# Performance work log

Hardware: AMD Instinct MI355X
Metric: run time of the kernel (lower is better)

The kernel has to match this reference:

```python
import jax, jax.numpy as jnp
import numpy as np

N = 50000      # num_nodes
E = 800000     # num_edges (before self-loops)
IN = 512       # in_channels
HID = 64       # hidden_channels
H = 8          # num_heads (layer 1)
OUT = 128      # out_channels
NEG_SLOPE = 0.2


def setup_inputs() -> dict:
    key = jax.random.key(0)
    ks = jax.random.split(key, 10)
    x = jax.random.normal(ks[0], (N, IN), jnp.float32)
    edge_index = jax.random.randint(ks[1], (2, E), 0, N, jnp.int32)

    def glorot(k, shape):
        fan_in, fan_out = shape[0], int(np.prod(shape[1:]))
        s = jnp.sqrt(2.0 / (fan_in + fan_out)).astype(jnp.float32)
        return jax.random.normal(k, shape, jnp.float32) * s

    # layer 1: GATConv(IN -> HID, heads=H, concat=True)
    W1 = glorot(ks[2], (IN, H * HID))
    att_src1 = glorot(ks[3], (H, HID))
    att_dst1 = glorot(ks[4], (H, HID))
    b1 = jnp.zeros((H * HID,), jnp.float32)
    # layer 2: GATConv(H*HID -> OUT, heads=1, concat=False)
    W2 = glorot(ks[5], (H * HID, OUT))
    att_src2 = glorot(ks[6], (1, OUT))
    att_dst2 = glorot(ks[7], (1, OUT))
    b2 = jnp.zeros((OUT,), jnp.float32)
    return {"x": x, "edge_index": edge_index,
            "W1": W1, "b1": b1, "att_src1": att_src1, "att_dst1": att_dst1,
            "W2": W2, "b2": b2, "att_src2": att_src2, "att_dst2": att_dst2}


def gat_layer(x, src, dst, W, b, a_src, a_dst, heads, concat):
    n = x.shape[0]
    h = (x @ W).reshape(n, heads, -1)                     # [N, H, C]
    e_src = (h * a_src).sum(-1)                           # [N, H]
    e_dst = (h * a_dst).sum(-1)                           # [N, H]
    e = jax.nn.leaky_relu(e_src[src] + e_dst[dst], NEG_SLOPE)   # [E, H]
    # segment softmax over incoming edges of each destination node
    m = jax.ops.segment_max(e, dst, num_segments=n)       # [N, H]
    m = jnp.where(jnp.isneginf(m), 0.0, m)                # empty segments
    p = jnp.exp(e - m[dst])                               # [E, H]
    s = jax.ops.segment_sum(p, dst, num_segments=n)       # [N, H]
    alpha = p / (s[dst] + 1e-16)                          # [E, H]
    out = jax.ops.segment_sum(alpha[..., None] * h[src], dst, num_segments=n)  # [N, H, C]
    if concat:
        return out.reshape(n, -1) + b
    return out.mean(axis=1) + b


def reference(x, edge_index, W1, b1, att_src1, att_dst1, W2, b2, att_src2, att_dst2):
    # PyG GATConv adds self-loops by default
    loops = jnp.arange(N, dtype=edge_index.dtype)
    src = jnp.concatenate([edge_index[0], loops])
    dst = jnp.concatenate([edge_index[1], loops])
    h = gat_layer(x, src, dst, W1, b1, att_src1, att_dst1, H, True)   # [N, H*HID]
    h = jax.nn.relu(h)
    out = gat_layer(h, src, dst, W2, b2, att_src2, att_dst2, 1, False)  # [N, OUT]
    return out
```

## Files before the change

### kernel.cpp

```cpp
#include <hip/hip_runtime.h>
#include <hip/hip_fp16.h>

#define NNODES 50000
#define NEDGES 800000
#define ETOT   (NNODES + NEDGES)
#define NH     8
#define HID    64
#define D1     512
#define INC    512
#define OUTC   128
#define NEG    0.2f
#define MPAD   50048

typedef __attribute__((ext_vector_type(8))) short short8;
typedef __attribute__((ext_vector_type(4))) float f32x4;
typedef _Float16 half8v __attribute__((ext_vector_type(8)));
typedef _Float16 half2v __attribute__((ext_vector_type(2)));

__device__ __forceinline__ ushort f2h_bits(float x) {
    _Float16 h = (_Float16)x; return __builtin_bit_cast(ushort, h);
}
__device__ __forceinline__ float h2f(ushort b) {
    return (float)__builtin_bit_cast(_Float16, b);
}
__device__ __forceinline__ uint splat_h2(float p) {
    uint b = (uint)f2h_bits(p); return b | (b << 16);
}
__device__ __forceinline__ half2v as_h2(uint u) { return __builtin_bit_cast(half2v, u); }
__device__ __forceinline__ float leaky(float v) { return v >= 0.f ? v : NEG * v; }

__global__ void count_deg(const int* __restrict__ ei, int* __restrict__ deg) {
    int i = blockIdx.x * 256 + threadIdx.x;
    if (i >= ETOT) return;
    int dst = (i < NEDGES) ? ei[NEDGES + i] : (i - NEDGES);
    atomicAdd(&deg[dst], 1);
}

__global__ void scan_deg(const int* __restrict__ deg, int* __restrict__ rs) {
    __shared__ int part[1024];
    const int n = NNODES;
    const int CH = (n + 1023) / 1024;
    int t = threadIdx.x;
    int lo = t * CH, hi = min(lo + CH, n);
    int s = 0;
    for (int i = lo; i < hi; ++i) s += deg[i];
    part[t] = s;
    __syncthreads();
    for (int off = 1; off < 1024; off <<= 1) {
        int v = (t >= off) ? part[t - off] : 0;
        __syncthreads();
        part[t] += v;
        __syncthreads();
    }
    int run = (t == 0) ? 0 : part[t - 1];
    for (int i = lo; i < hi; ++i) { rs[i] = run; run += deg[i]; }
    if (hi == n) rs[n] = run;
}

__global__ void scatter_edges(const int* __restrict__ ei, int* __restrict__ cursor,
                              int* __restrict__ csr_src) {
    int i = blockIdx.x * 256 + threadIdx.x;
    if (i >= ETOT) return;
    int src, dst;
    if (i < NEDGES) { src = ei[i]; dst = ei[NEDGES + i]; }
    else            { src = dst = i - NEDGES; }
    int pos = atomicAdd(&cursor[dst], 1);
    csr_src[pos] = src;
}

__global__ void cast_f16(const float* __restrict__ x, ushort* __restrict__ xh, int n4) {
    int i = blockIdx.x * 256 + threadIdx.x;
    if (i >= n4) return;
    float4 v = *(const float4*)&x[(size_t)i * 4];
    ushort4 o = { f2h_bits(v.x), f2h_bits(v.y), f2h_bits(v.z), f2h_bits(v.w) };
    *(ushort4*)&xh[(size_t)i * 4] = o;
}

__global__ void cast_wT(const float* __restrict__ W, ushort* __restrict__ WT, int K, int N) {
    int idx = blockIdx.x * 256 + threadIdx.x;
    if (idx >= K * N) return;
    int n = idx / K, k = idx - n * K;
    WT[idx] = f2h_bits(W[(size_t)k * N + n]);
}

template<int KDIM>
__global__ __launch_bounds__(256) void gemm1_f16(const ushort* __restrict__ A,
                                                 const ushort* __restrict__ Bt,
                                                 ushort* __restrict__ C,
                                                 const float* __restrict__ a_src,
                                                 const float* __restrict__ a_dst,
                                                 float* __restrict__ es,
                                                 float* __restrict__ ed,
                                                 int M, int N) {
    __shared__ __align__(16) ushort Asl[128 * 64];
    __shared__ __align__(16) ushort Bsl[128 * 64];
    const int tid  = threadIdx.x;
    const int lane = tid & 63;
    const int wid  = tid >> 6;
    const int wr   = wid >> 1, wc = wid & 1;
    const int fr   = lane & 15, fq = lane >> 4;
    const int m0   = blockIdx.x * 128;
    const int n0   = blockIdx.y * 128;

    f32x4 acc[4][4] = {};
    const int gcol = (((lane & 7) ^ ((lane >> 3) & 7))) * 8;

    for (int k0 = 0; k0 < KDIM; k0 += 64) {
        __syncthreads();
        #pragma unroll
        for (int i = 0; i < 4; ++i) {
            int chunk = wid * 4 + i;
            int r = chunk * 8 + (lane >> 3);
            const ushort* ga = A  + (size_t)(m0 + r) * KDIM + k0 + gcol;
            const ushort* gb = Bt + (size_t)(n0 + r) * KDIM + k0 + gcol;
            __builtin_amdgcn_global_load_lds(
                (const __attribute__((address_space(1))) void*)ga,
                (__attribute__((address_space(3))) void*)(Asl + chunk * 512), 16, 0, 0);
            __builtin_amdgcn_global_load_lds(
                (const __attribute__((address_space(1))) void*)gb,
                (__attribute__((address_space(3))) void*)(Bsl + chunk * 512), 16, 0, 0);
        }
        __syncthreads();
        #pragma unroll
        for (int ks = 0; ks < 2; ++ks) {
            short8 a[4], b[4];
            #pragma unroll
            for (int m = 0; m < 4; ++m) {
                int row = wr * 64 + m * 16 + fr;
                int slot = (ks * 4 + fq) ^ (fr & 7);
                a[m] = *(const short8*)&Asl[row * 64 + slot * 8];
            }
            #pragma unroll
            for (int n = 0; n < 4; ++n) {
                int row = wc * 64 + n * 16 + fr;
                int slot = (ks * 4 + fq) ^ (fr & 7);
                b[n] = *(const short8*)&Bsl[row * 64 + slot * 8];
            }
            #pragma unroll
            for (int m = 0; m < 4; ++m)
                #pragma unroll
                for (int n = 0; n < 4; ++n)
                    acc[m][n] = __builtin_amdgcn_mfma_f32_16x16x32_f16(
                        __builtin_bit_cast(half8v, a[m]),
                        __builtin_bit_cast(half8v, b[n]), acc[m][n], 0, 0, 0);
        }
    }
    #pragma unroll
    for (int m = 0; m < 4; ++m) {
        #pragma unroll
        for (int r = 0; r < 4; ++r) {
            int row = m0 + wr * 64 + m * 16 + fq * 4 + r;
            if (row >= M) continue;
            #pragma unroll
            for (int n = 0; n < 4; ++n)
                C[(size_t)row * N + n0 + wc * 64 + n * 16 + fr] = f2h_bits(acc[m][n][r]);
        }
    }
    {
        int h = (n0 + wc * 64) >> 6;
        float as[4], ad[4];
        #pragma unroll
        for (int n = 0; n < 4; ++n) {
            as[n] = a_src[h * HID + n * 16 + fr];
            ad[n] = a_dst[h * HID + n * 16 + fr];
        }
        #pragma unroll
        for (int m = 0; m < 4; ++m) {
            #pragma unroll
            for (int r = 0; r < 4; ++r) {
                float s = 0.f, d = 0.f;
                #pragma unroll
                for (int n = 0; n < 4; ++n) {
                    float v = acc[m][n][r];
                    s += v * as[n];
                    d += v * ad[n];
                }
                #pragma unroll
                for (int off = 1; off < 16; off <<= 1) {
                    s += __shfl_xor(s, off);
                    d += __shfl_xor(d, off);
                }
                if (fr == 0) {
                    int row = m0 + wr * 64 + m * 16 + fq * 4 + r;
                    if (row < M) {
                        es[row * NH + h] = s;
                        ed[row * NH + h] = d;
                    }
                }
            }
        }
    }
}

template<int KDIM>
__global__ __launch_bounds__(256) void gemm2_f16(const ushort* __restrict__ A,
                                                 const ushort* __restrict__ Bt,
                                                 ushort* __restrict__ C,
                                                 int M, int N) {
    __shared__ __align__(16) ushort Asl[64 * 64];
    __shared__ __align__(16) ushort Bsl[128 * 64];
    const int tid  = threadIdx.x;
    const int lane = tid & 63;
    const int wid  = tid >> 6;
    const int wr   = wid >> 1, wc = wid & 1;
    const int fr   = lane & 15, fq = lane >> 4;
    const int m0   = blockIdx.x * 64;
    const int n0   = blockIdx.y * 128;

    f32x4 acc[2][4] = {};
    const int gcol = (((lane & 7) ^ ((lane >> 3) & 7))) * 8;

    for (int k0 = 0; k0 < KDIM; k0 += 64) {
        __syncthreads();
        #pragma unroll
        for (int i = 0; i < 2; ++i) {
            int chunk = wid * 2 + i;
            int r = chunk * 8 + (lane >> 3);
            const ushort* ga = A + (size_t)(m0 + r) * KDIM + k0 + gcol;
            __builtin_amdgcn_global_load_lds(
                (const __attribute__((address_space(1))) void*)ga,
                (__attribute__((address_space(3))) void*)(Asl + chunk * 512), 16, 0, 0);
        }
        #pragma unroll
        for (int i = 0; i < 4; ++i) {
            int chunk = wid * 4 + i;
            int r = chunk * 8 + (lane >> 3);
            const ushort* gb = Bt + (size_t)(n0 + r) * KDIM + k0 + gcol;
            __builtin_amdgcn_global_load_lds(
                (const __attribute__((address_space(1))) void*)gb,
                (__attribute__((address_space(3))) void*)(Bsl + chunk * 512), 16, 0, 0);
        }
        __syncthreads();
        #pragma unroll
        for (int ks = 0; ks < 2; ++ks) {
            short8 a[2], b[4];
            #pragma unroll
            for (int m = 0; m < 2; ++m) {
                int row = wr * 32 + m * 16 + fr;
                int slot = (ks * 4 + fq) ^ (fr & 7);
                a[m] = *(const short8*)&Asl[row * 64 + slot * 8];
            }
            #pragma unroll
            for (int n = 0; n < 4; ++n) {
                int row = wc * 64 + n * 16 + fr;
                int slot = (ks * 4 + fq) ^ (fr & 7);
                b[n] = *(const short8*)&Bsl[row * 64 + slot * 8];
            }
            #pragma unroll
            for (int m = 0; m < 2; ++m)
                #pragma unroll
                for (int n = 0; n < 4; ++n)
                    acc[m][n] = __builtin_amdgcn_mfma_f32_16x16x32_f16(
                        __builtin_bit_cast(half8v, a[m]),
                        __builtin_bit_cast(half8v, b[n]), acc[m][n], 0, 0, 0);
        }
    }
    #pragma unroll
    for (int m = 0; m < 2; ++m) {
        #pragma unroll
        for (int r = 0; r < 4; ++r) {
            int row = m0 + wr * 32 + m * 16 + fq * 4 + r;
            if (row >= M) continue;
            #pragma unroll
            for (int n = 0; n < 4; ++n)
                C[(size_t)row * N + n0 + wc * 64 + n * 16 + fr] = f2h_bits(acc[m][n][r]);
        }
    }
}

__global__ void dots2(const ushort* __restrict__ h2, const float* __restrict__ a_src,
                      const float* __restrict__ a_dst,
                      float* __restrict__ es, float* __restrict__ ed) {
    int gw   = (blockIdx.x * blockDim.x + threadIdx.x) >> 6;
    int lane = threadIdx.x & 63;
    if (gw >= NNODES) return;
    uint u = *(const uint*)&h2[(size_t)gw * OUTC + lane * 2];
    float x0 = h2f((ushort)(u & 0xffffu)), x1 = h2f((ushort)(u >> 16));
    float s = x0 * a_src[lane * 2] + x1 * a_src[lane * 2 + 1];
    float d = x0 * a_dst[lane * 2] + x1 * a_dst[lane * 2 + 1];
    #pragma unroll
    for (int off = 1; off < 64; off <<= 1) {
        s += __shfl_xor(s, off);
        d += __shfl_xor(d, off);
    }
    if (lane == 0) { es[gw] = s; ed[gw] = d; }
}

#define CAP1 128
__global__ __launch_bounds__(256) void attn1(const ushort* __restrict__ h1,
                                             const float* __restrict__ esrc,
                                             const float* __restrict__ edst,
                                             const int* __restrict__ rs,
                                             const int* __restrict__ csr_src,
                                             const float* __restrict__ b1,
                                             ushort* __restrict__ out1) {
    int t = threadIdx.x, lane = t & 63, w = t >> 6;
    int n = blockIdx.x * 4 + w;
    int beg = rs[n], deg = rs[n + 1] - beg;
    int dcap = min(deg, CAP1);
    __shared__ uint  alpha_sh[4][CAP1][9];
    __shared__ int   ssrc_sh[4][CAP1];
    uint (*alpha)[9] = alpha_sh[w];
    int* ss = ssrc_sh[w];

    for (int e = lane; e < dcap; e += 64) ss[e] = csr_src[beg + e];

    float4 edA = *(const float4*)&edst[n * NH];
    float4 edB = *(const float4*)&edst[n * NH + 4];
    float mx[8], sm[8];
    #pragma unroll
    for (int h = 0; h < 8; ++h) { mx[h] = -1e30f; sm[h] = 0.f; }

    for (int e = lane; e < deg; e += 64) {
        int s = (e < CAP1) ? ss[e] : csr_src[beg + e];
        float4 eA = *(const float4*)&esrc[(size_t)s * NH];
        float4 eB = *(const float4*)&esrc[(size_t)s * NH + 4];
        float v[8] = { leaky(eA.x + edA.x), leaky(eA.y + edA.y),
                       leaky(eA.z + edA.z), leaky(eA.w + edA.w),
                       leaky(eB.x + edB.x), leaky(eB.y + edB.y),
                       leaky(eB.z + edB.z), leaky(eB.w + edB.w) };
        #pragma unroll
        for (int h = 0; h < 8; ++h) {
            if (e < CAP1) alpha[e][h] = __float_as_uint(v[h]);
            mx[h] = fmaxf(mx[h], v[h]);
        }
    }
    #pragma unroll
    for (int off = 1; off < 64; off <<= 1)
        #pragma unroll
        for (int h = 0; h < 8; ++h)
            mx[h] = fmaxf(mx[h], __shfl_xor(mx[h], off));

    for (int e = lane; e < deg; e += 64) {
        float v[8];
        if (e < CAP1) {
            #pragma unroll
            for (int h = 0; h < 8; ++h) v[h] = __uint_as_float(alpha[e][h]);
        } else {
            int s = csr_src[beg + e];
            float4 eA = *(const float4*)&esrc[(size_t)s * NH];
            float4 eB = *(const float4*)&esrc[(size_t)s * NH + 4];
            v[0] = leaky(eA.x + edA.x); v[1] = leaky(eA.y + edA.y);
            v[2] = leaky(eA.z + edA.z); v[3] = leaky(eA.w + edA.w);
            v[4] = leaky(eB.x + edB.x); v[5] = leaky(eB.y + edB.y);
            v[6] = leaky(eB.z + edB.z); v[7] = leaky(eB.w + edB.w);
        }
        #pragma unroll
        for (int h = 0; h < 8; ++h) {
            float p = __expf(v[h] - mx[h]);
            if (e < CAP1) alpha[e][h] = splat_h2(p);
            sm[h] += p;
        }
    }
    #pragma unroll
    for (int off = 1; off < 64; off <<= 1)
        #pragma unroll
        for (int h = 0; h < 8; ++h)
            sm[h] += __shfl_xor(sm[h], off);

    int h = lane >> 3;
    float mm = mx[0], ssv = sm[0], edn = edA.x;
    float edv[8] = { edA.x, edA.y, edA.z, edA.w, edB.x, edB.y, edB.z, edB.w };
    #pragma unroll
    for (int hh = 1; hh < 8; ++hh)
        if (h == hh) { mm = mx[hh]; ssv = sm[hh]; edn = edv[hh]; }
    float ri = 1.f / (ssv + 1e-16f);

    int c0 = lane * 8;
    half2v aA0 = {}, aA1 = {}, aA2 = {}, aA3 = {};
    half2v aB0 = {}, aB1 = {}, aB2 = {}, aB3 = {};
    int e = 0;
    for (; e + 2 <= dcap; e += 2) {
        int s0i = ss[e], s1i = ss[e + 1];
        uint4 u0 = *(const uint4*)&h1[(size_t)s0i * D1 + c0];
        uint4 u1 = *(const uint4*)&h1[(size_t)s1i * D1 + c0];
        half2v p0 = as_h2(alpha[e][h]);
        half2v p1 = as_h2(alpha[e + 1][h]);
        aA0 = as_h2(u0.x) * p0 + aA0; aA1 = as_h2(u0.y) * p0 + aA1;
        aA2 = as_h2(u0.z) * p0 + aA2; aA3 = as_h2(u0.w) * p0 + aA3;
        aB0 = as_h2(u1.x) * p1 + aB0; aB1 = as_h2(u1.y) * p1 + aB1;
        aB2 = as_h2(u1.z) * p1 + aB2; aB3 = as_h2(u1.w) * p1 + aB3;
    }
    for (; e < dcap; ++e) {
        int s = ss[e];
        uint4 u = *(const uint4*)&h1[(size_t)s * D1 + c0];
        half2v p = as_h2(alpha[e][h]);
        aA0 = as_h2(u.x) * p + aA0; aA1 = as_h2(u.y) * p + aA1;
        aA2 = as_h2(u.z) * p + aA2; aA3 = as_h2(u.w) * p + aA3;
    }
    for (; e < deg; ++e) {
        int s = csr_src[beg + e];
        float p = __expf(leaky(esrc[(size_t)s * NH + h] + edn) - mm);
        half2v ph = as_h2(splat_h2(p));
        uint4 u = *(const uint4*)&h1[(size_t)s * D1 + c0];
        aA0 = as_h2(u.x) * ph + aA0; aA1 = as_h2(u.y) * ph + aA1;
        aA2 = as_h2(u.z) * ph + aA2; aA3 = as_h2(u.w) * ph + aA3;
    }
    float4 bb0 = *(const float4*)&b1[c0];
    float4 bb1 = *(const float4*)&b1[c0 + 4];
    float o0 = fmaxf(((float)aA0[0] + (float)aB0[0]) * ri + bb0.x, 0.f);
    float o1 = fmaxf(((float)aA0[1] + (float)aB0[1]) * ri + bb0.y, 0.f);
    float o2 = fmaxf(((float)aA1[0] + (float)aB1[0]) * ri + bb0.z, 0.f);
    float o3 = fmaxf(((float)aA1[1] + (float)aB1[1]) * ri + bb0.w, 0.f);
    float o4 = fmaxf(((float)aA2[0] + (float)aB2[0]) * ri + bb1.x, 0.f);
    float o5 = fmaxf(((float)aA2[1] + (float)aB2[1]) * ri + bb1.y, 0.f);
    float o6 = fmaxf(((float)aA3[0] + (float)aB3[0]) * ri + bb1.z, 0.f);
    float o7 = fmaxf(((float)aA3[1] + (float)aB3[1]) * ri + bb1.w, 0.f);
    uint4 pk;
    pk.x = (uint)f2h_bits(o0) | ((uint)f2h_bits(o1) << 16);
    pk.y = (uint)f2h_bits(o2) | ((uint)f2h_bits(o3) << 16);
    pk.z = (uint)f2h_bits(o4) | ((uint)f2h_bits(o5) << 16);
    pk.w = (uint)f2h_bits(o6) | ((uint)f2h_bits(o7) << 16);
    *(uint4*)&out1[(size_t)n * D1 + c0] = pk;
}

#define CAP2 128
__global__ __launch_bounds__(256) void attn2(const ushort* __restrict__ h2,
                                             const float* __restrict__ esrc,
                                             const float* __restrict__ edst,
                                             const int* __restrict__ rs,
                                             const int* __restrict__ csr_src,
                                             const float* __restrict__ b2,
                                             float* __restrict__ out) {
    int t = threadIdx.x;
    int g = t >> 5, lane32 = t & 31;
    int n = blockIdx.x * 8 + g;
    if (n >= NNODES) return;
    int beg = rs[n], deg = rs[n + 1] - beg;
    int dcap = min(deg, CAP2);
    __shared__ float al_sh[8][CAP2];
    __shared__ int   ss_sh[8][CAP2];
    float* al = al_sh[g];
    int*   ss = ss_sh[g];

    for (int e = lane32; e < dcap; e += 32) ss[e] = csr_src[beg + e];

    float edn = edst[n];
    float m = -1e30f;
    for (int e = lane32; e < deg; e += 32) {
        int s = (e < CAP2) ? ss[e] : csr_src[beg + e];
        float v = leaky(esrc[s] + edn);
        if (e < CAP2) al[e] = v;
        m = fmaxf(m, v);
    }
    #pragma unroll
    for (int off = 16; off; off >>= 1) m = fmaxf(m, __shfl_xor(m, off));
    float ssum = 0.f;
    for (int e = lane32; e < deg; e += 32) {
        float v = (e < CAP2) ? al[e] : leaky(esrc[csr_src[beg + e]] + edn);
        float p = __expf(v - m);
        if (e < CAP2) *(uint*)&al[e] = splat_h2(p);
        ssum += p;
    }
    #pragma unroll
    for (int off = 16; off; off >>= 1) ssum += __shfl_xor(ssum, off);
    float ri = 1.f / (ssum + 1e-16f);

    int c0 = lane32 * 4;
    half2v a01 = {}, a01b = {}, a23 = {}, a23b = {};
    int e = 0;
    for (; e + 4 <= dcap; e += 4) {
        int s0i = ss[e], s1i = ss[e + 1], s2i = ss[e + 2], s3i = ss[e + 3];
        uint2 u0 = *(const uint2*)&h2[(size_t)s0i * OUTC + c0];
        uint2 u1 = *(const uint2*)&h2[(size_t)s1i * OUTC + c0];
        uint2 u2 = *(const uint2*)&h2[(size_t)s2i * OUTC + c0];
        uint2 u3 = *(const uint2*)&h2[(size_t)s3i * OUTC + c0];
        half2v p0 = as_h2(*(const uint*)&al[e]);
        half2v p1 = as_h2(*(const uint*)&al[e + 1]);
        half2v p2 = as_h2(*(const uint*)&al[e + 2]);
        half2v p3 = as_h2(*(const uint*)&al[e + 3]);
        a01  = as_h2(u0.x) * p0 + a01;  a23  = as_h2(u0.y) * p0 + a23;
        a01b = as_h2(u1.x) * p1 + a01b; a23b = as_h2(u1.y) * p1 + a23b;
        a01  = as_h2(u2.x) * p2 + a01;  a23  = as_h2(u2.y) * p2 + a23;
        a01b = as_h2(u3.x) * p3 + a01b; a23b = as_h2(u3.y) * p3 + a23b;
    }
    for (; e < dcap; ++e) {
        int s = ss[e];
        uint2 u = *(const uint2*)&h2[(size_t)s * OUTC + c0];
        half2v p = as_h2(*(const uint*)&al[e]);
        a01 = as_h2(u.x) * p + a01;
        a23 = as_h2(u.y) * p + a23;
    }
    for (; e < deg; ++e) {
        int s = csr_src[beg + e];
        float p = __expf(leaky(esrc[s] + edn) - m);
        half2v ph = as_h2(splat_h2(p));
        uint2 u = *(const uint2*)&h2[(size_t)s * OUTC + c0];
        a01 = as_h2(u.x) * ph + a01;
        a23 = as_h2(u.y) * ph + a23;
    }
    float4 bb = *(const float4*)&b2[c0];
    float4 o;
    o.x = ((float)a01[0] + (float)a01b[0]) * ri + bb.x;
    o.y = ((float)a01[1] + (float)a01b[1]) * ri + bb.y;
    o.z = ((float)a23[0] + (float)a23b[0]) * ri + bb.z;
    o.w = ((float)a23[1] + (float)a23b[1]) * ri + bb.w;
    *(float4*)&out[(size_t)n * OUTC + c0] = o;
}

extern "C" void kernel_launch(void* const* d_in, const int* in_sizes, int n_in,
                              void* d_out, int out_size, void* d_ws, size_t ws_size,
                              hipStream_t stream) {
    const float* x   = (const float*)d_in[0];
    const int*   ei  = (const int*)  d_in[1];
    const float* W1  = (const float*)d_in[2];
    const float* b1  = (const float*)d_in[3];
    const float* as1 = (const float*)d_in[4];
    const float* ad1 = (const float*)d_in[5];
    const float* W2  = (const float*)d_in[6];
    const float* b2  = (const float*)d_in[7];
    const float* as2 = (const float*)d_in[8];
    const float* ad2 = (const float*)d_in[9];
    float* out = (float*)d_out;

    char* ws = (char*)d_ws;
    size_t off = 0;
    auto alloc = [&](size_t bytes) -> void* {
        void* p = ws + off;
        off = (off + bytes + 255) & ~(size_t)255;
        return p;
    };
    ushort* xh    = (ushort*)alloc((size_t)MPAD * INC * 2);
    ushort* w1t   = (ushort*)alloc((size_t)D1 * INC * 2);
    ushort* w2t   = (ushort*)alloc((size_t)OUTC * D1 * 2);
    ushort* h1h   = (ushort*)alloc((size_t)MPAD * D1 * 2);
    ushort* out1h = (ushort*)alloc((size_t)MPAD * D1 * 2);
    ushort* h2h   = (ushort*)alloc((size_t)MPAD * OUTC * 2);
    float*  es1   = (float*)alloc((size_t)NNODES * NH * 4);
    float*  ed1   = (float*)alloc((size_t)NNODES * NH * 4);
    float*  es2   = (float*)alloc((size_t)NNODES * 4);
    float*  ed2   = (float*)alloc((size_t)NNODES * 4);
    int*    deg   = (int*)alloc((size_t)NNODES * 4);
    int*    rs    = (int*)alloc((size_t)(NNODES + 1) * 4);
    int*    cur   = (int*)alloc((size_t)NNODES * 4);
    int*    csr   = (int*)alloc((size_t)ETOT * 4);

    hipMemsetAsync(deg, 0, (size_t)NNODES * 4, stream);
    count_deg<<<(ETOT + 255) / 256, 256, 0, stream>>>(ei, deg);
    scan_deg<<<1, 1024, 0, stream>>>(deg, rs);
    hipMemcpyAsync(cur, rs, (size_t)NNODES * 4, hipMemcpyDeviceToDevice, stream);
    scatter_edges<<<(ETOT + 255) / 256, 256, 0, stream>>>(ei, cur, csr);

    cast_f16<<<(NNODES * INC / 4 + 255) / 256, 256, 0, stream>>>(x, xh, NNODES * INC / 4);
    cast_wT<<<(INC * D1 + 255) / 256, 256, 0, stream>>>(W1, w1t, INC, D1);
    cast_wT<<<(D1 * OUTC + 255) / 256, 256, 0, stream>>>(W2, w2t, D1, OUTC);

    gemm1_f16<INC><<<dim3(MPAD / 128, D1 / 128), 256, 0, stream>>>(
        xh, w1t, h1h, as1, ad1, es1, ed1, NNODES, D1);
    attn1<<<NNODES / 4, 256, 0, stream>>>(h1h, es1, ed1, rs, csr, b1, out1h);

    gemm2_f16<D1><<<dim3(MPAD / 64, OUTC / 128), 256, 0, stream>>>(out1h, w2t, h2h, NNODES, OUTC);
    dots2<<<(NNODES * 64 + 255) / 256, 256, 0, stream>>>(h2h, as2, ad2, es2, ed2);
    attn2<<<NNODES / 8, 256, 0, stream>>>(h2h, es2, ed2, rs, csr, b2, out);
}
```

Measured before the change: 596.1 us.

## Drop softmax max pass, fuse layer-2 dots into GEMM, widen attention gathers

Removes the max-reduction pass from both segment softmaxes by exponentiating logits directly and pre-normalizing alphas in shared memory. Fuses the layer-2 attention dot products into the gemm2 epilogue via atomics after zeroing the buffers, removes a device copy by writing the cursor in the scan, unrolls the attn1 gather to four edges, and reworks attn2 to 16 lanes per node with 16-byte loads. Skipping the max subtraction risks overflow for large logits, and the atomics add nondeterminism.

```diff
diff --git a/kernel.cpp b/kernel.cpp
--- a/kernel.cpp
+++ b/kernel.cpp
@@ -36,7 +36,8 @@
     atomicAdd(&deg[dst], 1);
 }
 
-__global__ void scan_deg(const int* __restrict__ deg, int* __restrict__ rs) {
+__global__ void scan_deg(const int* __restrict__ deg, int* __restrict__ rs,
+                         int* __restrict__ cur) {
     __shared__ int part[1024];
     const int n = NNODES;
     const int CH = (n + 1023) / 1024;
@@ -53,7 +54,7 @@
         __syncthreads();
     }
     int run = (t == 0) ? 0 : part[t - 1];
-    for (int i = lo; i < hi; ++i) { rs[i] = run; run += deg[i]; }
+    for (int i = lo; i < hi; ++i) { rs[i] = run; cur[i] = run; run += deg[i]; }
     if (hi == n) rs[n] = run;
 }
 
@@ -196,6 +197,10 @@
 __global__ __launch_bounds__(256) void gemm2_f16(const ushort* __restrict__ A,
                                                  const ushort* __restrict__ Bt,
                                                  ushort* __restrict__ C,
+                                                 const float* __restrict__ a_src,
+                                                 const float* __restrict__ a_dst,
+                                                 float* __restrict__ es,
+                                                 float* __restrict__ ed,
                                                  int M, int N) {
     __shared__ __align__(16) ushort Asl[64 * 64];
     __shared__ __align__(16) ushort Bsl[128 * 64];
@@ -266,24 +271,40 @@
                 C[(size_t)row * N + n0 + wc * 64 + n * 16 + fr] = f2h_bits(acc[m][n][r]);
         }
     }
-}
-
-__global__ void dots2(const ushort* __restrict__ h2, const float* __restrict__ a_src,
-                      const float* __restrict__ a_dst,
-                      float* __restrict__ es, float* __restrict__ ed) {
-    int gw   = (blockIdx.x * blockDim.x + threadIdx.x) >> 6;
-    int lane = threadIdx.x & 63;
-    if (gw >= NNODES) return;
-    uint u = *(const uint*)&h2[(size_t)gw * OUTC + lane * 2];
-    float x0 = h2f((ushort)(u & 0xffffu)), x1 = h2f((ushort)(u >> 16));
-    float s = x0 * a_src[lane * 2] + x1 * a_src[lane * 2 + 1];
-    float d = x0 * a_dst[lane * 2] + x1 * a_dst[lane * 2 + 1];
-    #pragma unroll
-    for (int off = 1; off < 64; off <<= 1) {
-        s += __shfl_xor(s, off);
-        d += __shfl_xor(d, off);
-    }
-    if (lane == 0) { es[gw] = s; ed[gw] = d; }
+    {
+        int cb = n0 + wc * 64;
+        float as[4], ad[4];
+        #pragma unroll
+        for (int n = 0; n < 4; ++n) {
+            as[n] = a_src[cb + n * 16 + fr];
+            ad[n] = a_dst[cb + n * 16 + fr];
+        }
+        #pragma unroll
+        for (int m = 0; m < 2; ++m) {
+            #pragma unroll
+            for (int r = 0; r < 4; ++r) {
+                float s = 0.f, d = 0.f;
+                #pragma unroll
+                for (int n = 0; n < 4; ++n) {
+                    float v = acc[m][n][r];
+                    s += v * as[n];
+                    d += v * ad[n];
+                }
+                #pragma unroll
+                for (int off = 1; off < 16; off <<= 1) {
+                    s += __shfl_xor(s, off);
+                    d += __shfl_xor(d, off);
+                }
+                if (fr == 0) {
+                    int row = m0 + wr * 32 + m * 16 + fq * 4 + r;
+                    if (row < M) {
+                        atomicAdd(&es[row], s);
+                        atomicAdd(&ed[row], d);
+                    }
+                }
+            }
+        }
+    }
 }
 
 #define CAP1 128
@@ -307,79 +328,79 @@
 
     float4 edA = *(const float4*)&edst[n * NH];
     float4 edB = *(const float4*)&edst[n * NH + 4];
-    float mx[8], sm[8];
-    #pragma unroll
-    for (int h = 0; h < 8; ++h) { mx[h] = -1e30f; sm[h] = 0.f; }
+    float sm0 = 0.f, sm1 = 0.f, sm2 = 0.f, sm3 = 0.f;
+    float sm4 = 0.f, sm5 = 0.f, sm6 = 0.f, sm7 = 0.f;
 
     for (int e = lane; e < deg; e += 64) {
         int s = (e < CAP1) ? ss[e] : csr_src[beg + e];
         float4 eA = *(const float4*)&esrc[(size_t)s * NH];
         float4 eB = *(const float4*)&esrc[(size_t)s * NH + 4];
-        float v[8] = { leaky(eA.x + edA.x), leaky(eA.y + edA.y),
-                       leaky(eA.z + edA.z), leaky(eA.w + edA.w),
-                       leaky(eB.x + edB.x), leaky(eB.y + edB.y),
-                       leaky(eB.z + edB.z), leaky(eB.w + edB.w) };
-        #pragma unroll
-        for (int h = 0; h < 8; ++h) {
-            if (e < CAP1) alpha[e][h] = __float_as_uint(v[h]);
-            mx[h] = fmaxf(mx[h], v[h]);
-        }
+        float p0 = __expf(leaky(eA.x + edA.x));
+        float p1 = __expf(leaky(eA.y + edA.y));
+        float p2 = __expf(leaky(eA.z + edA.z));
+        float p3 = __expf(leaky(eA.w + edA.w));
+        float p4 = __expf(leaky(eB.x + edB.x));
+        float p5 = __expf(leaky(eB.y + edB.y));
+        float p6 = __expf(leaky(eB.z + edB.z));
+        float p7 = __expf(leaky(eB.w + edB.w));
+        if (e < CAP1) {
+            alpha[e][0] = __float_as_uint(p0); alpha[e][1] = __float_as_uint(p1);
+            alpha[e][2] = __float_as_uint(p2); alpha[e][3] = __float_as_uint(p3);
+            alpha[e][4] = __float_as_uint(p4); alpha[e][5] = __float_as_uint(p5);
+            alpha[e][6] = __float_as_uint(p6); alpha[e][7] = __float_as_uint(p7);
+        }
+        sm0 += p0; sm1 += p1; sm2 += p2; sm3 += p3;
+        sm4 += p4; sm5 += p5; sm6 += p6; sm7 += p7;
     }
     #pragma unroll
-    for (int off = 1; off < 64; off <<= 1)
-        #pragma unroll
-        for (int h = 0; h < 8; ++h)
-            mx[h] = fmaxf(mx[h], __shfl_xor(mx[h], off));
-
-    for (int e = lane; e < deg; e += 64) {
-        float v[8];
-        if (e < CAP1) {
-            #pragma unroll
-            for (int h = 0; h < 8; ++h) v[h] = __uint_as_float(alpha[e][h]);
-        } else {
-            int s = csr_src[beg + e];
-            float4 eA = *(const float4*)&esrc[(size_t)s * NH];
-            float4 eB = *(const float4*)&esrc[(size_t)s * NH + 4];
-            v[0] = leaky(eA.x + edA.x); v[1] = leaky(eA.y + edA.y);
-            v[2] = leaky(eA.z + edA.z); v[3] = leaky(eA.w + edA.w);
-            v[4] = leaky(eB.x + edB.x); v[5] = leaky(eB.y + edB.y);
-            v[6] = leaky(eB.z + edB.z); v[7] = leaky(eB.w + edB.w);
-        }
-        #pragma unroll
-        for (int h = 0; h < 8; ++h) {
-            float p = __expf(v[h] - mx[h]);
-            if (e < CAP1) alpha[e][h] = splat_h2(p);
-            sm[h] += p;
-        }
-    }
-    #pragma unroll
-    for (int off = 1; off < 64; off <<= 1)
-        #pragma unroll
-        for (int h = 0; h < 8; ++h)
-            sm[h] += __shfl_xor(sm[h], off);
+    for (int off = 1; off < 64; off <<= 1) {
+        sm0 += __shfl_xor(sm0, off); sm1 += __shfl_xor(sm1, off);
+        sm2 += __shfl_xor(sm2, off); sm3 += __shfl_xor(sm3, off);
+        sm4 += __shfl_xor(sm4, off); sm5 += __shfl_xor(sm5, off);
+        sm6 += __shfl_xor(sm6, off); sm7 += __shfl_xor(sm7, off);
+    }
+    float ri0 = 1.f / (sm0 + 1e-16f), ri1 = 1.f / (sm1 + 1e-16f);
+    float ri2 = 1.f / (sm2 + 1e-16f), ri3 = 1.f / (sm3 + 1e-16f);
+    float ri4 = 1.f / (sm4 + 1e-16f), ri5 = 1.f / (sm5 + 1e-16f);
+    float ri6 = 1.f / (sm6 + 1e-16f), ri7 = 1.f / (sm7 + 1e-16f);
+
+    #define NORM(H, RI) \
+        for (int e = lane; e < dcap; e += 64) \
+            alpha[e][H] = splat_h2(__uint_as_float(alpha[e][H]) * RI);
+    NORM(0, ri0) NORM(1, ri1) NORM(2, ri2) NORM(3, ri3)
+    NORM(4, ri4) NORM(5, ri5) NORM(6, ri6) NORM(7, ri7)
+    #undef NORM
 
     int h = lane >> 3;
-    float mm = mx[0], ssv = sm[0], edn = edA.x;
+    float riv[8] = { ri0, ri1, ri2, ri3, ri4, ri5, ri6, ri7 };
     float edv[8] = { edA.x, edA.y, edA.z, edA.w, edB.x, edB.y, edB.z, edB.w };
+    float rih = riv[0], edn = edv[0];
     #pragma unroll
     for (int hh = 1; hh < 8; ++hh)
-        if (h == hh) { mm = mx[hh]; ssv = sm[hh]; edn = edv[hh]; }
-    float ri = 1.f / (ssv + 1e-16f);
+        if (h == hh) { rih = riv[hh]; edn = edv[hh]; }
 
     int c0 = lane * 8;
     half2v aA0 = {}, aA1 = {}, aA2 = {}, aA3 = {};
     half2v aB0 = {}, aB1 = {}, aB2 = {}, aB3 = {};
     int e = 0;
-    for (; e + 2 <= dcap; e += 2) {
-        int s0i = ss[e], s1i = ss[e + 1];
+    for (; e + 4 <= dcap; e += 4) {
+        int s0i = ss[e], s1i = ss[e + 1], s2i = ss[e + 2], s3i = ss[e + 3];
         uint4 u0 = *(const uint4*)&h1[(size_t)s0i * D1 + c0];
         uint4 u1 = *(const uint4*)&h1[(size_t)s1i * D1 + c0];
+        uint4 u2 = *(const uint4*)&h1[(size_t)s2i * D1 + c0];
+        uint4 u3 = *(const uint4*)&h1[(size_t)s3i * D1 + c0];
         half2v p0 = as_h2(alpha[e][h]);
         half2v p1 = as_h2(alpha[e + 1][h]);
+        half2v p2 = as_h2(alpha[e + 2][h]);
+        half2v p3 = as_h2(alpha[e + 3][h]);
         aA0 = as_h2(u0.x) * p0 + aA0; aA1 = as_h2(u0.y) * p0 + aA1;
         aA2 = as_h2(u0.z) * p0 + aA2; aA3 = as_h2(u0.w) * p0 + aA3;
         aB0 = as_h2(u1.x) * p1 + aB0; aB1 = as_h2(u1.y) * p1 + aB1;
         aB2 = as_h2(u1.z) * p1 + aB2; aB3 = as_h2(u1.w) * p1 + aB3;
+        aA0 = as_h2(u2.x) * p2 + aA0; aA1 = as_h2(u2.y) * p2 + aA1;
+        aA2 = as_h2(u2.z) * p2 + aA2; aA3 = as_h2(u2.w) * p2 + aA3;
+        aB0 = as_h2(u3.x) * p3 + aB0; aB1 = as_h2(u3.y) * p3 + aB1;
+        aB2 = as_h2(u3.z) * p3 + aB2; aB3 = as_h2(u3.w) * p3 + aB3;
     }
     for (; e < dcap; ++e) {
         int s = ss[e];
@@ -390,7 +411,7 @@
     }
     for (; e < deg; ++e) {
         int s = csr_src[beg + e];
-        float p = __expf(leaky(esrc[(size_t)s * NH + h] + edn) - mm);
+        float p = __expf(leaky(esrc[(size_t)s * NH + h] + edn)) * rih;
         half2v ph = as_h2(splat_h2(p));
         uint4 u = *(const uint4*)&h1[(size_t)s * D1 + c0];
         aA0 = as_h2(u.x) * ph + aA0; aA1 = as_h2(u.y) * ph + aA1;
@@ -398,14 +419,14 @@
     }
     float4 bb0 = *(const float4*)&b1[c0];
     float4 bb1 = *(const float4*)&b1[c0 + 4];
-    float o0 = fmaxf(((float)aA0[0] + (float)aB0[0]) * ri + bb0.x, 0.f);
-    float o1 = fmaxf(((float)aA0[1] + (float)aB0[1]) * ri + bb0.y, 0.f);
-    float o2 = fmaxf(((float)aA1[0] + (float)aB1[0]) * ri + bb0.z, 0.f);
-    float o3 = fmaxf(((float)aA1[1] + (float)aB1[1]) * ri + bb0.w, 0.f);
-    float o4 = fmaxf(((float)aA2[0] + (float)aB2[0]) * ri + bb1.x, 0.f);
-    float o5 = fmaxf(((float)aA2[1] + (float)aB2[1]) * ri + bb1.y, 0.f);
-    float o6 = fmaxf(((float)aA3[0] + (float)aB3[0]) * ri + bb1.z, 0.f);
-    float o7 = fmaxf(((float)aA3[1] + (float)aB3[1]) * ri + bb1.w, 0.f);
+    float o0 = fmaxf(((float)aA0[0] + (float)aB0[0]) + bb0.x, 0.f);
+    float o1 = fmaxf(((float)aA0[1] + (float)aB0[1]) + bb0.y, 0.f);
+    float o2 = fmaxf(((float)aA1[0] + (float)aB1[0]) + bb0.z, 0.f);
+    float o3 = fmaxf(((float)aA1[1] + (float)aB1[1]) + bb0.w, 0.f);
+    float o4 = fmaxf(((float)aA2[0] + (float)aB2[0]) + bb1.x, 0.f);
+    float o5 = fmaxf(((float)aA2[1] + (float)aB2[1]) + bb1.y, 0.f);
+    float o6 = fmaxf(((float)aA3[0] + (float)aB3[0]) + bb1.z, 0.f);
+    float o7 = fmaxf(((float)aA3[1] + (float)aB3[1]) + bb1.w, 0.f);
     uint4 pk;
     pk.x = (uint)f2h_bits(o0) | ((uint)f2h_bits(o1) << 16);
     pk.y = (uint)f2h_bits(o2) | ((uint)f2h_bits(o3) << 16);
@@ -423,79 +444,75 @@
                                              const float* __restrict__ b2,
                                              float* __restrict__ out) {
     int t = threadIdx.x;
-    int g = t >> 5, lane32 = t & 31;
-    int n = blockIdx.x * 8 + g;
-    if (n >= NNODES) return;
+    int g = t >> 4, lane16 = t & 15;
+    int n = blockIdx.x * 16 + g;
     int beg = rs[n], deg = rs[n + 1] - beg;
     int dcap = min(deg, CAP2);
-    __shared__ float al_sh[8][CAP2];
-    __shared__ int   ss_sh[8][CAP2];
-    float* al = al_sh[g];
-    int*   ss = ss_sh[g];
-
-    for (int e = lane32; e < dcap; e += 32) ss[e] = csr_src[beg + e];
+    __shared__ uint al_sh[16][CAP2];
+    __shared__ int  ss_sh[16][CAP2];
+    uint* al = al_sh[g];
+    int*  ss = ss_sh[g];
+
+    for (int e = lane16; e < dcap; e += 16) ss[e] = csr_src[beg + e];
 
     float edn = edst[n];
-    float m = -1e30f;
-    for (int e = lane32; e < deg; e += 32) {
+    float ssum = 0.f;
+    for (int e = lane16; e < deg; e += 16) {
         int s = (e < CAP2) ? ss[e] : csr_src[beg + e];
-        float v = leaky(esrc[s] + edn);
-        if (e < CAP2) al[e] = v;
-        m = fmaxf(m, v);
+        float p = __expf(leaky(esrc[s] + edn));
+        if (e < CAP2) al[e] = __float_as_uint(p);
+        ssum += p;
     }
     #pragma unroll
-    for (int off = 16; off; off >>= 1) m = fmaxf(m, __shfl_xor(m, off));
-    float ssum = 0.f;
-    for (int e = lane32; e < deg; e += 32) {
-        float v = (e < CAP2) ? al[e] : leaky(esrc[csr_src[beg + e]] + edn);
-        float p = __expf(v - m);
-        if (e < CAP2) *(uint*)&al[e] = splat_h2(p);
-        ssum += p;
-    }
-    #pragma unroll
-    for (int off = 16; off; off >>= 1) ssum += __shfl_xor(ssum, off);
+    for (int off = 1; off < 16; off <<= 1) ssum += __shfl_xor(ssum, off);
     float ri = 1.f / (ssum + 1e-16f);
 
-    int c0 = lane32 * 4;
-    half2v a01 = {}, a01b = {}, a23 = {}, a23b = {};
+    for (int e = lane16; e < dcap; e += 16)
+        al[e] = splat_h2(__uint_as_float(al[e]) * ri);
+
+    int c0 = lane16 * 8;
+    half2v aA0 = {}, aA1 = {}, aA2 = {}, aA3 = {};
+    half2v aB0 = {}, aB1 = {}, aB2 = {}, aB3 = {};
     int e = 0;
-    for (; e + 4 <= dcap; e += 4) {
-        int s0i = ss[e], s1i = ss[e + 1], s2i = ss[e + 2], s3i = ss[e + 3];
-        uint2 u0 = *(const uint2*)&h2[(size_t)s0i * OUTC + c0];
-        uint2 u1 = *(const uint2*)&h2[(size_t)s1i * OUTC + c0];
-        uint2 u2 = *(const uint2*)&h2[(size_t)s2i * OUTC + c0];
-        uint2 u3 = *(const uint2*)&h2[(size_t)s3i * OUTC + c0];
-        half2v p0 = as_h2(*(const uint*)&al[e]);
-        half2v p1 = as_h2(*(const uint*)&al[e + 1]);
-        half2v p2 = as_h2(*(const uint*)&al[e + 2]);
-        half2v p3 = as_h2(*(const uint*)&al[e + 3]);
-        a01  = as_h2(u0.x) * p0 + a01;  a23  = as_h2(u0.y) * p0 + a23;
-        a01b = as_h2(u1.x) * p1 + a01b; a23b = as_h2(u1.y) * p1 + a23b;
-        a01  = as_h2(u2.x) * p2 + a01;  a23  = as_h2(u2.y) * p2 + a23;
-        a01b = as_h2(u3.x) * p3 + a01b; a23b = as_h2(u3.y) * p3 + a23b;
+    for (; e + 2 <= dcap; e += 2) {
+        int s0i = ss[e], s1i = ss[e + 1];
+        uint4 u0 = *(const uint4*)&h2[(size_t)s0i * OUTC + c0];
+        uint4 u1 = *(const uint4*)&h2[(size_t)s1i * OUTC + c0];
+        half2v p0 = as_h2(al[e]);
+        half2v p1 = as_h2(al[e + 1]);
+        aA0 = as_h2(u0.x) * p0 + aA0; aA1 = as_h2(u0.y) * p0 + aA1;
+        aA2 = as_h2(u0.z) * p0 + aA2; aA3 = as_h2(u0.w) * p0 + aA3;
+        aB0 = as_h2(u1.x) * p1 + aB0; aB1 = as_h2(u1.y) * p1 + aB1;
+        aB2 = as_h2(u1.z) * p1 + aB2; aB3 = as_h2(u1.w) * p1 + aB3;
     }
     for (; e < dcap; ++e) {
         int s = ss[e];
-        uint2 u = *(const uint2*)&h2[(size_t)s * OUTC + c0];
-        half2v p = as_h2(*(const uint*)&al[e]);
-        a01 = as_h2(u.x) * p + a01;
-        a23 = as_h2(u.y) * p + a23;
+        uint4 u = *(const uint4*)&h2[(size_t)s * OUTC + c0];
+        half2v p = as_h2(al[e]);
+        aA0 = as_h2(u.x) * p + aA0; aA1 = as_h2(u.y) * p + aA1;
+        aA2 = as_h2(u.z) * p + aA2; aA3 = as_h2(u.w) * p + aA3;
     }
     for (; e < deg; ++e) {
         int s = csr_src[beg + e];
-        float p = __expf(leaky(esrc[s] + edn) - m);
+        float p = __expf(leaky(esrc[s] + edn)) * ri;
         half2v ph = as_h2(splat_h2(p));
-        uint2 u = *(const uint2*)&h2[(size_t)s * OUTC + c0];
-        a01 = as_h2(u.x) * ph + a01;
-        a23 = as_h2(u.y) * ph + a23;
-    }
-    float4 bb = *(const float4*)&b2[c0];
-    float4 o;
-    o.x = ((float)a01[0] + (float)a01b[0]) * ri + bb.x;
-    o.y = ((float)a01[1] + (float)a01b[1]) * ri + bb.y;
-    o.z = ((float)a23[0] + (float)a23b[0]) * ri + bb.z;
-    o.w = ((float)a23[1] + (float)a23b[1]) * ri + bb.w;
-    *(float4*)&out[(size_t)n * OUTC + c0] = o;
+        uint4 u = *(const uint4*)&h2[(size_t)s * OUTC + c0];
+        aA0 = as_h2(u.x) * ph + aA0; aA1 = as_h2(u.y) * ph + aA1;
+        aA2 = as_h2(u.z) * ph + aA2; aA3 = as_h2(u.w) * ph + aA3;
+    }
+    float4 bb0 = *(const float4*)&b2[c0];
+    float4 bb1 = *(const float4*)&b2[c0 + 4];
+    float4 oA, oB;
+    oA.x = ((float)aA0[0] + (float)aB0[0]) + bb0.x;
+    oA.y = ((float)aA0[1] + (float)aB0[1]) + bb0.y;
+    oA.z = ((float)aA1[0] + (float)aB1[0]) + bb0.z;
+    oA.w = ((float)aA1[1] + (float)aB1[1]) + bb0.w;
+    oB.x = ((float)aA2[0] + (float)aB2[0]) + bb1.x;
+    oB.y = ((float)aA2[1] + (float)aB2[1]) + bb1.y;
+    oB.z = ((float)aA3[0] + (float)aB3[0]) + bb1.z;
+    oB.w = ((float)aA3[1] + (float)aB3[1]) + bb1.w;
+    *(float4*)&out[(size_t)n * OUTC + c0] = oA;
+    *(float4*)&out[(size_t)n * OUTC + c0 + 4] = oB;
 }
 
 extern "C" void kernel_launch(void* const* d_in, const int* in_sizes, int n_in,
@@ -537,19 +554,20 @@
 
     hipMemsetAsync(deg, 0, (size_t)NNODES * 4, stream);
     count_deg<<<(ETOT + 255) / 256, 256, 0, stream>>>(ei, deg);
-    scan_deg<<<1, 1024, 0, stream>>>(deg, rs);
-    hipMemcpyAsync(cur, rs, (size_t)NNODES * 4, hipMemcpyDeviceToDevice, stream);
+    scan_deg<<<1, 1024, 0, stream>>>(deg, rs, cur);
     scatter_edges<<<(ETOT + 255) / 256, 256, 0, stream>>>(ei, cur, csr);
 
     cast_f16<<<(NNODES * INC / 4 + 255) / 256, 256, 0, stream>>>(x, xh, NNODES * INC / 4);
     cast_wT<<<(INC * D1 + 255) / 256, 256, 0, stream>>>(W1, w1t, INC, D1);
     cast_wT<<<(D1 * OUTC + 255) / 256, 256, 0, stream>>>(W2, w2t, D1, OUTC);
+    hipMemsetAsync(es2, 0, (size_t)((char*)csr - (char*)es2) > 0 ?
+                   (size_t)((char*)deg - (char*)es2) : 0, stream);
 
     gemm1_f16<INC><<<dim3(MPAD / 128, D1 / 128), 256, 0, stream>>>(
         xh, w1t, h1h, as1, ad1, es1, ed1, NNODES, D1);
     attn1<<<NNODES / 4, 256, 0, stream>>>(h1h, es1, ed1, rs, csr, b1, out1h);
 
-    gemm2_f16<D1><<<dim3(MPAD / 64, OUTC / 128), 256, 0, stream>>>(out1h, w2t, h2h, NNODES, OUTC);
-    dots2<<<(NNODES * 64 + 255) / 256, 256, 0, stream>>>(h2h, as2, ad2, es2, ed2);
-    attn2<<<NNODES / 8, 256, 0, stream>>>(h2h, es2, ed2, rs, csr, b2, out);
-}
+    gemm2_f16<D1><<<dim3(MPAD / 64, OUTC / 128), 256, 0, stream>>>(
+        out1h, w2t, h2h, as2, ad2, es2, ed2, NNODES, OUTC);
+    attn2<<<NNODES / 16, 256, 0, stream>>>(h2h, es2, ed2, rs, csr, b2, out);
+}
```

New measurement: 615.7 us. 1.03x slower.
